# Optimization experiments

Measured on AMD Instinct MI355X. Metric: run time of the kernel, lower is better.

The kernel has to match this reference:

```python
import jax, jax.numpy as jnp
import numpy as np
import math

EPS = 1e-5

def _ln(x, g, b):
    m = jnp.mean(x, axis=-1, keepdims=True)
    v = jnp.mean((x - m) ** 2, axis=-1, keepdims=True)
    return (x - m) * jax.lax.rsqrt(v + EPS) * g + b

def _heads(t, H):
    B, T, C = t.shape
    return t.reshape(B, T, H, C // H).transpose(0, 2, 1, 3)  # [B,H,T,D]

def _merge(t):
    B, H, T, D = t.shape
    return t.transpose(0, 2, 1, 3).reshape(B, T, H * D)

def _self_attn(x, w, b, pw, pb, H):
    B, T, C = x.shape
    q, k, v = jnp.split(x @ w + b, 3, axis=-1)
    q, k, v = _heads(q, H), _heads(k, H), _heads(v, H)
    D = C // H
    att = jnp.einsum('bhqd,bhkd->bhqk', q, k) * (1.0 / math.sqrt(D))
    causal = jnp.tril(jnp.ones((T, T), bool))
    att = jnp.where(causal[None, None], att, jnp.float32(-jnp.inf))
    att = jax.nn.softmax(att, axis=-1)
    out = _merge(jnp.einsum('bhqk,bhkd->bhqd', att, v))
    return out @ pw + pb

def _cross_attn(enc, dec, w, b, pw, pb, H):
    B, Td, C = dec.shape
    q_dec = jnp.split(dec @ w + b, 3, axis=-1)[0]
    _, k_enc, v_enc = jnp.split(enc @ w + b, 3, axis=-1)
    q = _heads(q_dec, H); k = _heads(k_enc, H); v = _heads(v_enc, H)
    D = C // H
    att = jnp.einsum('bhqd,bhkd->bhqk', q, k) * (1.0 / math.sqrt(D))
    att = jax.nn.softmax(att, axis=-1)
    out = _merge(jnp.einsum('bhqk,bhkd->bhqd', att, v))
    return out @ pw + pb

def _block(x, encoder_embd,
           ln1_g, ln1_b, ln2_g, ln2_b, ln3_g, ln3_b,
           attn_w, attn_b, aproj_w, aproj_b,
           ca_w, ca_b, caproj_w, caproj_b,
           fc_w, fc_b, mproj_w, mproj_b,
           down_w, down_b, up_w, up_b, H=16):
    x = x + _self_attn(_ln(x, ln1_g, ln1_b), attn_w, attn_b, aproj_w, aproj_b, H)
    x = x + _cross_attn(encoder_embd, _ln(x, ln2_g, ln2_b), ca_w, ca_b, caproj_w, caproj_b, H)
    h = jax.nn.gelu(_ln(x, ln3_g, ln3_b) @ fc_w + fc_b, approximate=True) @ mproj_w + mproj_b
    adapt = jax.nn.gelu(h @ down_w + down_b, approximate=True) @ up_w + up_b + h  # Adapter residual
    return x + adapt


def setup_inputs() -> dict:
    key = jax.random.key(0)
    ks = jax.random.split(key, 12)
    B, T, Te, C, H = 4, 1024, 257, 1024, 16
    s = 0.02
    f32 = jnp.float32
    return {
        'x': jax.random.normal(ks[0], (B, T, C), f32),
        'encoder_embd': jax.random.normal(ks[1], (B, Te, C), f32),
        'prefix_embd': jnp.zeros((B, 1, C), f32),
        'ln1_g': jnp.ones((C,), f32), 'ln1_b': jnp.zeros((C,), f32),
        'ln2_g': jnp.ones((C,), f32), 'ln2_b': jnp.zeros((C,), f32),
        'ln3_g': jnp.ones((C,), f32), 'ln3_b': jnp.zeros((C,), f32),
        'attn_w': jax.random.normal(ks[2], (C, 3 * C), f32) * s,
        'attn_b': jnp.zeros((3 * C,), f32),
        'aproj_w': jax.random.normal(ks[3], (C, C), f32) * s,
        'aproj_b': jnp.zeros((C,), f32),
        'ca_w': jax.random.normal(ks[4], (C, 3 * C), f32) * s,
        'ca_b': jnp.zeros((3 * C,), f32),
        'caproj_w': jax.random.normal(ks[5], (C, C), f32) * s,
        'caproj_b': jnp.zeros((C,), f32),
        'fc_w': jax.random.normal(ks[6], (C, 4 * C), f32) * s,
        'fc_b': jnp.zeros((4 * C,), f32),
        'mproj_w': jax.random.normal(ks[7], (4 * C, C), f32) * s,
        'mproj_b': jnp.zeros((C,), f32),
        'down_w': jax.random.normal(ks[8], (C, C // 4), f32) * s,
        'down_b': jnp.zeros((C // 4,), f32),
        'up_w': jax.random.normal(ks[9], (C // 4, C), f32) * s,
        'up_b': jnp.zeros((C,), f32),
    }


def reference(x, encoder_embd, prefix_embd,
              ln1_g, ln1_b, ln2_g, ln2_b, ln3_g, ln3_b,
              attn_w, attn_b, aproj_w, aproj_b,
              ca_w, ca_b, caproj_w, caproj_b,
              fc_w, fc_b, mproj_w, mproj_b,
              down_w, down_b, up_w, up_b):
    # prefix_embd unused (peft='adapter')
    return _block(x, encoder_embd,
                  ln1_g, ln1_b, ln2_g, ln2_b, ln3_g, ln3_b,
                  attn_w, attn_b, aproj_w, aproj_b,
                  ca_w, ca_b, caproj_w, caproj_b,
                  fc_w, fc_b, mproj_w, mproj_b,
                  down_w, down_b, up_w, up_b)
```

## Files before the change

kernel.cpp:

```cpp
#include <hip/hip_runtime.h>

typedef __attribute__((ext_vector_type(8))) short short8v;
typedef __attribute__((ext_vector_type(8))) unsigned short ushort8v;
typedef __attribute__((ext_vector_type(4))) float f32x4;

__device__ __forceinline__ unsigned short f2b(float f) {
  unsigned int u = __float_as_uint(f);
  unsigned int r = (u + 0x7FFFu + ((u >> 16) & 1u)) >> 16;
  return (unsigned short)r;
}
__device__ __forceinline__ float b2f(unsigned short h) {
  return __uint_as_float(((unsigned int)h) << 16);
}
__device__ __forceinline__ float gelu_f(float x) {
  float z = 0.7978845608028654f * (x + 0.044715f * x * x * x);
  float e = __expf(2.0f * z);
  float t = 1.0f - 2.0f / (e + 1.0f);
  return 0.5f * x * (1.0f + t);
}
__device__ __forceinline__ void gload16(const void* g, void* l) {
  __builtin_amdgcn_global_load_lds((const __attribute__((address_space(1))) unsigned int*)g,
                                   (__attribute__((address_space(3))) unsigned int*)l,
                                   16, 0, 0);
}

__global__ __launch_bounds__(256) void k_transpose_cvt(const float* __restrict__ w,
                                                       unsigned short* __restrict__ wt,
                                                       int K, int N) {
  __shared__ float tile[64][65];
  int tn = blockIdx.x * 64, tk = blockIdx.y * 64;
  int c = threadIdx.x & 63, r0 = threadIdx.x >> 6;
#pragma unroll
  for (int p = 0; p < 16; ++p) {
    int r = r0 + p * 4;
    tile[r][c] = w[(size_t)(tk + r) * N + tn + c];
  }
  __syncthreads();
#pragma unroll
  for (int p = 0; p < 16; ++p) {
    int r = r0 + p * 4;
    wt[(size_t)(tn + r) * K + tk + c] = f2b(tile[c][r]);
  }
}

__global__ void k_cvt_bf16(const float* __restrict__ in, unsigned short* __restrict__ out, int n) {
  int i = blockIdx.x * 256 + threadIdx.x;
  if (i < n) out[i] = f2b(in[i]);
}

__global__ __launch_bounds__(256) void k_ln(const float* __restrict__ in,
                                            const float* __restrict__ g,
                                            const float* __restrict__ b,
                                            unsigned short* __restrict__ out) {
  int row = blockIdx.x;
  const float* x = in + (size_t)row * 1024;
  int t = threadIdx.x;
  float v0 = x[t], v1 = x[t + 256], v2 = x[t + 512], v3 = x[t + 768];
  float s = v0 + v1 + v2 + v3;
  float s2 = v0 * v0 + v1 * v1 + v2 * v2 + v3 * v3;
#pragma unroll
  for (int m = 1; m < 64; m <<= 1) { s += __shfl_xor(s, m); s2 += __shfl_xor(s2, m); }
  __shared__ float rs[4], rs2[4];
  int w = t >> 6;
  if ((t & 63) == 0) { rs[w] = s; rs2[w] = s2; }
  __syncthreads();
  s = rs[0] + rs[1] + rs[2] + rs[3];
  s2 = rs2[0] + rs2[1] + rs2[2] + rs2[3];
  float mean = s * (1.0f / 1024.0f);
  float var = s2 * (1.0f / 1024.0f) - mean * mean;
  float rinv = rsqrtf(var + 1e-5f);
  unsigned short* o = out + (size_t)row * 1024;
  o[t]       = f2b((v0 - mean) * rinv * g[t]       + b[t]);
  o[t + 256] = f2b((v1 - mean) * rinv * g[t + 256] + b[t + 256]);
  o[t + 512] = f2b((v2 - mean) * rinv * g[t + 512] + b[t + 512]);
  o[t + 768] = f2b((v3 - mean) * rinv * g[t + 768] + b[t + 768]);
}

template <bool GELU>
__global__ __launch_bounds__(512, 2) void k_g256(
    const unsigned short* __restrict__ A, int lda,
    const unsigned short* __restrict__ W, int ldw,
    const float* __restrict__ bias,
    unsigned short* __restrict__ outB, int ldo, int K) {
  __shared__ unsigned short lds[65536];
  const int t = threadIdx.x;
  const int tileM = blockIdx.y * 256, tileN = blockIdx.x * 256;
  const int lane = t & 63, w = t >> 6;
  const int wm = w >> 2, wn = w & 3;
  const int lr16 = lane & 15, kc4 = lane >> 4;

  const int row1 = t >> 2, row2 = row1 + 128, cs = t & 3;
  const int c1 = (cs ^ ((row1 >> 1) & 3)) * 8;
  const int c2 = (cs ^ ((row2 >> 1) & 3)) * 8;
  const unsigned short* a1 = A + (size_t)(tileM + row1) * lda + c1;
  const unsigned short* a2 = A + (size_t)(tileM + row2) * lda + c2;
  const unsigned short* w1 = W + (size_t)(tileN + row1) * ldw + c1;
  const unsigned short* w2 = W + (size_t)(tileN + row2) * ldw + c2;

  f32x4 acc[8][4];
#pragma unroll
  for (int i = 0; i < 8; ++i)
#pragma unroll
    for (int j = 0; j < 4; ++j) acc[i][j] = f32x4{0.f, 0.f, 0.f, 0.f};

  const int nt = K >> 6;

#define STAGE256(b, koff)                                  \
  do {                                                     \
    unsigned short* dst = &lds[(b) * 32768 + t * 8];       \
    gload16(a1 + (koff), dst);                             \
    gload16(a2 + (koff), dst + 4096);                      \
    gload16(a1 + (koff) + 32, dst + 8192);                 \
    gload16(a2 + (koff) + 32, dst + 12288);                \
    gload16(w1 + (koff), dst + 16384);                     \
    gload16(w2 + (koff), dst + 20480);                     \
    gload16(w1 + (koff) + 32, dst + 24576);                \
    gload16(w2 + (koff) + 32, dst + 28672);                \
  } while (0)

  STAGE256(0, 0);
  asm volatile("s_waitcnt vmcnt(0)" ::: "memory");
  __builtin_amdgcn_s_barrier();

  for (int T = 0; T < nt; ++T) {
    if (T + 1 < nt) STAGE256((T + 1) & 1, (T + 1) * 64);
    const unsigned short* buf = &lds[(T & 1) * 32768];
#pragma unroll
    for (int s = 0; s < 2; ++s) {
      const unsigned short* ab = buf + s * 8192;
      const unsigned short* bb = buf + 16384 + s * 8192;
      short8v bfr[4];
#pragma unroll
      for (int n = 0; n < 4; ++n) {
        int r = wn * 64 + n * 16 + lr16;
        bfr[n] = *(const short8v*)&bb[r * 32 + (kc4 ^ ((r >> 1) & 3)) * 8];
      }
#pragma unroll
      for (int mi = 0; mi < 8; ++mi) {
        int r = wm * 128 + mi * 16 + lr16;
        short8v af = *(const short8v*)&ab[r * 32 + (kc4 ^ ((r >> 1) & 3)) * 8];
#pragma unroll
        for (int n = 0; n < 4; ++n)
          acc[mi][n] = __builtin_amdgcn_mfma_f32_16x16x32_bf16(af, bfr[n], acc[mi][n], 0, 0, 0);
      }
    }
    if (T + 1 < nt) {
      asm volatile("s_waitcnt vmcnt(0)" ::: "memory");
      __builtin_amdgcn_s_barrier();
    }
  }
#undef STAGE256

#pragma unroll
  for (int mi = 0; mi < 8; ++mi) {
#pragma unroll
    for (int n = 0; n < 4; ++n) {
      int col = tileN + wn * 64 + n * 16 + lr16;
      float bv = bias[col];
#pragma unroll
      for (int qi = 0; qi < 4; ++qi) {
        int row = tileM + wm * 128 + mi * 16 + kc4 * 4 + qi;
        float v = acc[mi][n][qi] + bv;
        if (GELU) v = gelu_f(v);
        outB[(size_t)row * ldo + col] = f2b(v);
      }
    }
  }
}

template <bool GELU, bool WF32, bool WBF16, int NRES>
__global__ __launch_bounds__(256) void k_g128(
    const unsigned short* __restrict__ A, int lda,
    const unsigned short* __restrict__ W, int ldw,
    const float* __restrict__ bias,
    const float* __restrict__ res1, const float* __restrict__ res2,
    float* __restrict__ outF, unsigned short* __restrict__ outB,
    int M, int N, int K) {
  __shared__ unsigned short lds[32768];
  const int t = threadIdx.x;
  const int tileM = blockIdx.y * 128, tileN = blockIdx.x * 128;
  const int lane = t & 63, w = t >> 6;
  const int wm = (w >> 1) * 64, wn = (w & 1) * 64;
  const int lr16 = lane & 15, kc4 = lane >> 4;

  const int row1 = t >> 2, row2 = row1 + 64, cs = t & 3;
  const int c1 = (cs ^ ((row1 >> 1) & 3)) * 8;
  const int c2 = (cs ^ ((row2 >> 1) & 3)) * 8;
  int gr1 = tileM + row1; if (gr1 >= M) gr1 = M - 1;
  int gr2 = tileM + row2; if (gr2 >= M) gr2 = M - 1;
  const unsigned short* a1 = A + (size_t)gr1 * lda + c1;
  const unsigned short* a2 = A + (size_t)gr2 * lda + c2;
  const unsigned short* w1 = W + (size_t)(tileN + row1) * ldw + c1;
  const unsigned short* w2 = W + (size_t)(tileN + row2) * ldw + c2;

  f32x4 acc[4][4];
#pragma unroll
  for (int i = 0; i < 4; ++i)
#pragma unroll
    for (int j = 0; j < 4; ++j) acc[i][j] = f32x4{0.f, 0.f, 0.f, 0.f};

  const int nt = K >> 6;

#define STAGE128(b, koff)                                  \
  do {                                                     \
    unsigned short* dst = &lds[(b) * 16384 + t * 8];       \
    gload16(a1 + (koff), dst);                             \
    gload16(a2 + (koff), dst + 2048);                      \
    gload16(a1 + (koff) + 32, dst + 4096);                 \
    gload16(a2 + (koff) + 32, dst + 6144);                 \
    gload16(w1 + (koff), dst + 8192);                      \
    gload16(w2 + (koff), dst + 10240);                     \
    gload16(w1 + (koff) + 32, dst + 12288);                \
    gload16(w2 + (koff) + 32, dst + 14336);                \
  } while (0)

  STAGE128(0, 0);
  asm volatile("s_waitcnt vmcnt(0)" ::: "memory");
  __builtin_amdgcn_s_barrier();

  for (int T = 0; T < nt; ++T) {
    if (T + 1 < nt) STAGE128((T + 1) & 1, (T + 1) * 64);
    const unsigned short* buf = &lds[(T & 1) * 16384];
#pragma unroll
    for (int s = 0; s < 2; ++s) {
      const unsigned short* ab = buf + s * 4096;
      const unsigned short* bb = buf + 8192 + s * 4096;
      short8v bfr[4];
#pragma unroll
      for (int n = 0; n < 4; ++n) {
        int r = wn + n * 16 + lr16;
        bfr[n] = *(const short8v*)&bb[r * 32 + (kc4 ^ ((r >> 1) & 3)) * 8];
      }
#pragma unroll
      for (int mi = 0; mi < 4; ++mi) {
        int r = wm + mi * 16 + lr16;
        short8v af = *(const short8v*)&ab[r * 32 + (kc4 ^ ((r >> 1) & 3)) * 8];
#pragma unroll
        for (int n = 0; n < 4; ++n)
          acc[mi][n] = __builtin_amdgcn_mfma_f32_16x16x32_bf16(af, bfr[n], acc[mi][n], 0, 0, 0);
      }
    }
    if (T + 1 < nt) {
      asm volatile("s_waitcnt vmcnt(0)" ::: "memory");
      __builtin_amdgcn_s_barrier();
    }
  }
#undef STAGE128

#pragma unroll
  for (int mi = 0; mi < 4; ++mi) {
#pragma unroll
    for (int n = 0; n < 4; ++n) {
      int col = tileN + wn + n * 16 + lr16;
      float bv = bias[col];
#pragma unroll
      for (int qi = 0; qi < 4; ++qi) {
        int row = tileM + wm + mi * 16 + kc4 * 4 + qi;
        if (row < M) {
          float v = acc[mi][n][qi] + bv;
          if (GELU) v = gelu_f(v);
          size_t o = (size_t)row * N + col;
          if (NRES >= 1) v += res1[o];
          if (NRES >= 2) v += res2[o];
          if (WF32) outF[o] = v;
          if (WBF16) outB[o] = f2b(v);
        }
      }
    }
  }
}

__global__ __launch_bounds__(256) void k_vtrans(const unsigned short* __restrict__ src,
                                                int src_stride, int src_off, int TB,
                                                unsigned short* __restrict__ dst, int dst_tstride) {
  __shared__ unsigned short tile[64][72];
  int tb = blockIdx.x, bh = blockIdx.y;
  int b = bh >> 4, h = bh & 15;
  int t = threadIdx.x;
  int r = t >> 2, c0 = (t & 3) * 16;
  int tok = tb * 64 + r; if (tok >= TB) tok = TB - 1;
  const unsigned short* s = src + (size_t)(b * TB + tok) * src_stride + src_off + h * 64 + c0;
  *(ushort8v*)&tile[r][c0] = *(const ushort8v*)s;
  *(ushort8v*)&tile[r][c0 + 8] = *(const ushort8v*)(s + 8);
  __syncthreads();
  unsigned short tmp[16];
#pragma unroll
  for (int j = 0; j < 16; ++j) tmp[j] = tile[c0 + j][r];
  unsigned short* dp = dst + ((size_t)bh * 64 + r) * dst_tstride + tb * 64 + c0;
  *(ushort8v*)dp = *(const ushort8v*)&tmp[0];
  *(ushort8v*)(dp + 8) = *(const ushort8v*)&tmp[8];
}

template <bool CAUSAL>
__global__ __launch_bounds__(256) void k_attn(
    const unsigned short* __restrict__ Qb, int q_stride,
    const unsigned short* __restrict__ Kb, int k_stride, int k_off, int TKR,
    const unsigned short* __restrict__ Vt, int vt_tstride,
    unsigned short* __restrict__ out, int Tk) {
  __shared__ unsigned short Kl[64 * 72];
  __shared__ unsigned short Vl[64 * 72];
  __shared__ unsigned short Pl[4][16 * 72];
  int qb = blockIdx.x, bh = blockIdx.y;
  int b = bh >> 4, h = bh & 15;
  int t = threadIdx.x, lane = t & 63, w = t >> 6;
  int g = lane >> 4, lc = lane & 15;

  int qrow_g = qb * 64 + w * 16 + lc;
  const unsigned short* qp = Qb + (size_t)(b * 1024 + qrow_g) * q_stride + h * 64 + g * 8;
  short8v aq0 = *(const short8v*)qp;
  short8v aq1 = *(const short8v*)(qp + 32);

  f32x4 o[4];
  float m_[4], l_[4];
#pragma unroll
  for (int dt = 0; dt < 4; ++dt) o[dt] = f32x4{0.f, 0.f, 0.f, 0.f};
#pragma unroll
  for (int r = 0; r < 4; ++r) { m_[r] = -3.0e38f; l_[r] = 0.0f; }

  int srow = t >> 2;
  int sc = (t & 3) * 16;
  int ntiles = CAUSAL ? (qb + 1) : ((Tk + 63) >> 6);

  for (int kt = 0; kt < ntiles; ++kt) {
    __syncthreads();
    {
      int kg = kt * 64 + srow;
      if (!CAUSAL && kg >= Tk) kg = Tk - 1;
      const unsigned short* ks = Kb + (size_t)(b * TKR + kg) * k_stride + k_off + h * 64 + sc;
      *(ushort8v*)&Kl[srow * 72 + sc]     = *(const ushort8v*)ks;
      *(ushort8v*)&Kl[srow * 72 + sc + 8] = *(const ushort8v*)(ks + 8);
      const unsigned short* vs = Vt + ((size_t)bh * 64 + srow) * vt_tstride + kt * 64 + sc;
      *(ushort8v*)&Vl[srow * 72 + sc]     = *(const ushort8v*)vs;
      *(ushort8v*)&Vl[srow * 72 + sc + 8] = *(const ushort8v*)(vs + 8);
    }
    __syncthreads();

    f32x4 s[4];
#pragma unroll
    for (int jt = 0; jt < 4; ++jt) {
      short8v bk0 = *(const short8v*)&Kl[(jt * 16 + lc) * 72 + g * 8];
      short8v bk1 = *(const short8v*)&Kl[(jt * 16 + lc) * 72 + g * 8 + 32];
      f32x4 acc = f32x4{0.f, 0.f, 0.f, 0.f};
      acc = __builtin_amdgcn_mfma_f32_16x16x32_bf16(aq0, bk0, acc, 0, 0, 0);
      acc = __builtin_amdgcn_mfma_f32_16x16x32_bf16(aq1, bk1, acc, 0, 0, 0);
      s[jt] = acc;
    }
#pragma unroll
    for (int jt = 0; jt < 4; ++jt)
#pragma unroll
      for (int r = 0; r < 4; ++r) {
        float sv = s[jt][r] * 0.125f;
        bool masked = CAUSAL ? (kt == qb && (jt * 16 + lc) > (w * 16 + g * 4 + r))
                             : (kt * 64 + jt * 16 + lc >= Tk);
        s[jt][r] = masked ? -3.0e38f : sv;
      }
    float f[4];
#pragma unroll
    for (int r = 0; r < 4; ++r) {
      float mx = fmaxf(fmaxf(s[0][r], s[1][r]), fmaxf(s[2][r], s[3][r]));
      mx = fmaxf(mx, __shfl_xor(mx, 1));
      mx = fmaxf(mx, __shfl_xor(mx, 2));
      mx = fmaxf(mx, __shfl_xor(mx, 4));
      mx = fmaxf(mx, __shfl_xor(mx, 8));
      float mnew = fmaxf(m_[r], mx);
      f[r] = __expf(m_[r] - mnew);
      m_[r] = mnew;
      float rsum = 0.0f;
#pragma unroll
      for (int jt = 0; jt < 4; ++jt) {
        float p = __expf(s[jt][r] - mnew);
        s[jt][r] = p;
        rsum += p;
      }
      rsum += __shfl_xor(rsum, 1);
      rsum += __shfl_xor(rsum, 2);
      rsum += __shfl_xor(rsum, 4);
      rsum += __shfl_xor(rsum, 8);
      l_[r] = l_[r] * f[r] + rsum;
    }
#pragma unroll
    for (int dt = 0; dt < 4; ++dt)
#pragma unroll
      for (int r = 0; r < 4; ++r) o[dt][r] *= f[r];
#pragma unroll
    for (int jt = 0; jt < 4; ++jt)
#pragma unroll
      for (int r = 0; r < 4; ++r)
        Pl[w][(g * 4 + r) * 72 + jt * 16 + lc] = f2b(s[jt][r]);
    short8v ap0 = *(const short8v*)&Pl[w][lc * 72 + g * 8];
    short8v ap1 = *(const short8v*)&Pl[w][lc * 72 + g * 8 + 32];
#pragma unroll
    for (int dt = 0; dt < 4; ++dt) {
      short8v bv0 = *(const short8v*)&Vl[(dt * 16 + lc) * 72 + g * 8];
      short8v bv1 = *(const short8v*)&Vl[(dt * 16 + lc) * 72 + g * 8 + 32];
      o[dt] = __builtin_amdgcn_mfma_f32_16x16x32_bf16(ap0, bv0, o[dt], 0, 0, 0);
      o[dt] = __builtin_amdgcn_mfma_f32_16x16x32_bf16(ap1, bv1, o[dt], 0, 0, 0);
    }
  }
  size_t orow = (size_t)(b * 1024 + qb * 64 + w * 16) * 1024 + h * 64;
#pragma unroll
  for (int r = 0; r < 4; ++r) {
    float inv = 1.0f / l_[r];
#pragma unroll
    for (int dt = 0; dt < 4; ++dt)
      out[orow + (size_t)(g * 4 + r) * 1024 + dt * 16 + lc] = f2b(o[dt][r] * inv);
  }
}

extern "C" void kernel_launch(void* const* d_in, const int* in_sizes, int n_in,
                              void* d_out, int out_size, void* d_ws, size_t ws_size,
                              hipStream_t stream) {
  (void)in_sizes; (void)n_in; (void)out_size; (void)ws_size;
  const float* x       = (const float*)d_in[0];
  const float* enc     = (const float*)d_in[1];
  const float* ln1_g   = (const float*)d_in[3];
  const float* ln1_b   = (const float*)d_in[4];
  const float* ln2_g   = (const float*)d_in[5];
  const float* ln2_b   = (const float*)d_in[6];
  const float* ln3_g   = (const float*)d_in[7];
  const float* ln3_b   = (const float*)d_in[8];
  const float* attn_w  = (const float*)d_in[9];
  const float* attn_b  = (const float*)d_in[10];
  const float* aproj_w = (const float*)d_in[11];
  const float* aproj_b = (const float*)d_in[12];
  const float* ca_w    = (const float*)d_in[13];
  const float* ca_b    = (const float*)d_in[14];
  const float* caproj_w= (const float*)d_in[15];
  const float* caproj_b= (const float*)d_in[16];
  const float* fc_w    = (const float*)d_in[17];
  const float* fc_b    = (const float*)d_in[18];
  const float* mproj_w = (const float*)d_in[19];
  const float* mproj_b = (const float*)d_in[20];
  const float* down_w  = (const float*)d_in[21];
  const float* down_b  = (const float*)d_in[22];
  const float* up_w    = (const float*)d_in[23];
  const float* up_b    = (const float*)d_in[24];
  float* out = (float*)d_out;
  char* ws = (char*)d_ws;

  const size_t O_WATTN = 0, O_WAPROJ = 6291456, O_WCA = 8388608, O_WCAPROJ = 14680064,
               O_WFC = 16777216, O_WMPROJ = 25165824, O_WDOWN = 33554432, O_WUP = 34078720,
               O_ENC = 34603008, O_LN = 36708352, O_BIG = 45096960,
               O_XRES = 78651392, O_HF = 95428608, O_ATTN = 112205824;

  unsigned short* wt_attn   = (unsigned short*)(ws + O_WATTN);
  unsigned short* wt_aproj  = (unsigned short*)(ws + O_WAPROJ);
  unsigned short* wt_ca     = (unsigned short*)(ws + O_WCA);
  unsigned short* wt_caproj = (unsigned short*)(ws + O_WCAPROJ);
  unsigned short* wt_fc     = (unsigned short*)(ws + O_WFC);
  unsigned short* wt_mproj  = (unsigned short*)(ws + O_WMPROJ);
  unsigned short* wt_down   = (unsigned short*)(ws + O_WDOWN);
  unsigned short* wt_up     = (unsigned short*)(ws + O_WUP);
  unsigned short* encbf     = (unsigned short*)(ws + O_ENC);
  unsigned short* lnout     = (unsigned short*)(ws + O_LN);
  unsigned short* hbf       = (unsigned short*)(ws + O_LN);
  unsigned short* qkvb      = (unsigned short*)(ws + O_BIG);
  unsigned short* vt_self   = (unsigned short*)(ws + O_BIG + 25165824);
  unsigned short* q2b       = (unsigned short*)(ws + O_BIG);
  unsigned short* kvb       = (unsigned short*)(ws + O_BIG + 8388608);
  unsigned short* vt_cross  = (unsigned short*)(ws + O_BIG + 12599296);
  unsigned short* caout     = (unsigned short*)(ws + O_BIG + 15220736);
  unsigned short* fcout     = (unsigned short*)(ws + O_BIG);
  float*          xres      = (float*)(ws + O_XRES);
  float*          hf        = (float*)(ws + O_HF);
  unsigned short* attnout   = (unsigned short*)(ws + O_ATTN);
  unsigned short* dmid      = (unsigned short*)(ws + O_ATTN);

  dim3 blk(256);
  dim3 blk5(512);

  k_transpose_cvt<<<dim3(48, 16), blk, 0, stream>>>(attn_w,  wt_attn,   1024, 3072);
  k_transpose_cvt<<<dim3(16, 16), blk, 0, stream>>>(aproj_w, wt_aproj,  1024, 1024);
  k_transpose_cvt<<<dim3(48, 16), blk, 0, stream>>>(ca_w,    wt_ca,     1024, 3072);
  k_transpose_cvt<<<dim3(16, 16), blk, 0, stream>>>(caproj_w,wt_caproj, 1024, 1024);
  k_transpose_cvt<<<dim3(64, 16), blk, 0, stream>>>(fc_w,    wt_fc,     1024, 4096);
  k_transpose_cvt<<<dim3(16, 64), blk, 0, stream>>>(mproj_w, wt_mproj,  4096, 1024);
  k_transpose_cvt<<<dim3(4, 16),  blk, 0, stream>>>(down_w,  wt_down,   1024, 256);
  k_transpose_cvt<<<dim3(16, 4),  blk, 0, stream>>>(up_w,    wt_up,     256,  1024);
  k_cvt_bf16<<<dim3(4112), blk, 0, stream>>>(enc, encbf, 1028 * 1024);

  k_ln<<<dim3(4096), blk, 0, stream>>>(x, ln1_g, ln1_b, lnout);
  k_g256<false><<<dim3(12, 16), blk5, 0, stream>>>(
      lnout, 1024, wt_attn, 1024, attn_b, qkvb, 3072, 1024);
  k_vtrans<<<dim3(16, 64), blk, 0, stream>>>(qkvb, 3072, 2048, 1024, vt_self, 1024);
  k_attn<true><<<dim3(16, 64), blk, 0, stream>>>(
      qkvb, 3072, qkvb, 3072, 1024, 1024, vt_self, 1024, attnout, 1024);
  k_g128<false, true, false, 1><<<dim3(8, 32), blk, 0, stream>>>(
      attnout, 1024, wt_aproj, 1024, aproj_b, x, nullptr, xres, nullptr, 4096, 1024, 1024);

  k_ln<<<dim3(4096), blk, 0, stream>>>(xres, ln2_g, ln2_b, lnout);
  k_g128<false, false, true, 0><<<dim3(8, 32), blk, 0, stream>>>(
      lnout, 1024, wt_ca, 1024, ca_b, nullptr, nullptr, nullptr, q2b, 4096, 1024, 1024);
  k_g128<false, false, true, 0><<<dim3(16, 9), blk, 0, stream>>>(
      encbf, 1024, wt_ca + (size_t)1024 * 1024, 1024, ca_b + 1024, nullptr, nullptr,
      nullptr, kvb, 1028, 2048, 1024);
  k_vtrans<<<dim3(5, 64), blk, 0, stream>>>(kvb, 2048, 1024, 257, vt_cross, 320);
  k_attn<false><<<dim3(16, 64), blk, 0, stream>>>(
      q2b, 1024, kvb, 2048, 0, 257, vt_cross, 320, caout, 257);
  k_g128<false, true, false, 1><<<dim3(8, 32), blk, 0, stream>>>(
      caout, 1024, wt_caproj, 1024, caproj_b, xres, nullptr, xres, nullptr, 4096, 1024, 1024);

  k_ln<<<dim3(4096), blk, 0, stream>>>(xres, ln3_g, ln3_b, lnout);
  k_g256<true><<<dim3(16, 16), blk5, 0, stream>>>(
      lnout, 1024, wt_fc, 1024, fc_b, fcout, 4096, 1024);
  k_g128<false, true, true, 0><<<dim3(8, 32), blk, 0, stream>>>(
      fcout, 4096, wt_mproj, 4096, mproj_b, nullptr, nullptr, hf, hbf, 4096, 1024, 4096);

  k_g128<true, false, true, 0><<<dim3(2, 32), blk, 0, stream>>>(
      hbf, 1024, wt_down, 1024, down_b, nullptr, nullptr, nullptr, dmid, 4096, 256, 1024);
  k_g128<false, true, false, 2><<<dim3(8, 32), blk, 0, stream>>>(
      dmid, 256, wt_up, 256, up_b, hf, xres, out, nullptr, 4096, 1024, 256);
}
```

Measured before the change: 504.9 us.

## Deepen k_g256 pipeline to half-tile stages and drop fp32 h buffer

```diff
diff --git a/kernel.cpp b/kernel.cpp
--- a/kernel.cpp
+++ b/kernel.cpp
@@ -77,7 +77,7 @@
 }
 
 template <bool GELU>
-__global__ __launch_bounds__(512, 2) void k_g256(
+__global__ __launch_bounds__(512, 2) void k_g256p(
     const unsigned short* __restrict__ A, int lda,
     const unsigned short* __restrict__ W, int ldw,
     const float* __restrict__ bias,
@@ -104,52 +104,67 @@
     for (int j = 0; j < 4; ++j) acc[i][j] = f32x4{0.f, 0.f, 0.f, 0.f};
 
   const int nt = K >> 6;
-
-#define STAGE256(b, koff)                                  \
-  do {                                                     \
-    unsigned short* dst = &lds[(b) * 32768 + t * 8];       \
-    gload16(a1 + (koff), dst);                             \
-    gload16(a2 + (koff), dst + 4096);                      \
-    gload16(a1 + (koff) + 32, dst + 8192);                 \
-    gload16(a2 + (koff) + 32, dst + 12288);                \
-    gload16(w1 + (koff), dst + 16384);                     \
-    gload16(w2 + (koff), dst + 20480);                     \
-    gload16(w1 + (koff) + 32, dst + 24576);                \
-    gload16(w2 + (koff) + 32, dst + 28672);                \
+  const int H = nt * 4;
+
+#define STAGE_HALF(h)                                                        \
+  do {                                                                       \
+    int tile_s = (h) >> 2, id = (h) & 3, slot = (h) & 7;                     \
+    int koff = tile_s * 64 + (id >> 1) * 32;                                 \
+    unsigned short* dst = &lds[slot * 8192 + t * 8];                         \
+    if (id & 1) { gload16(w1 + koff, dst); gload16(w2 + koff, dst + 4096); } \
+    else        { gload16(a1 + koff, dst); gload16(a2 + koff, dst + 4096); } \
   } while (0)
 
-  STAGE256(0, 0);
-  asm volatile("s_waitcnt vmcnt(0)" ::: "memory");
+#pragma unroll
+  for (int h = 0; h < 6; ++h) { if (h < H) STAGE_HALF(h); }
+  asm volatile("s_waitcnt vmcnt(8)" ::: "memory");
   __builtin_amdgcn_s_barrier();
 
   for (int T = 0; T < nt; ++T) {
-    if (T + 1 < nt) STAGE256((T + 1) & 1, (T + 1) * 64);
-    const unsigned short* buf = &lds[(T & 1) * 32768];
-#pragma unroll
-    for (int s = 0; s < 2; ++s) {
-      const unsigned short* ab = buf + s * 8192;
-      const unsigned short* bb = buf + 16384 + s * 8192;
-      short8v bfr[4];
-#pragma unroll
-      for (int n = 0; n < 4; ++n) {
-        int r = wn * 64 + n * 16 + lr16;
-        bfr[n] = *(const short8v*)&bb[r * 32 + (kc4 ^ ((r >> 1) & 3)) * 8];
-      }
-#pragma unroll
-      for (int mi = 0; mi < 8; ++mi) {
-        int r = wm * 128 + mi * 16 + lr16;
-        short8v af = *(const short8v*)&ab[r * 32 + (kc4 ^ ((r >> 1) & 3)) * 8];
+    short8v bfr[4];
+#pragma unroll
+    for (int q = 0; q < 4; ++q) {
+      const int ks = q >> 1, mh = q & 1;
+      const int aslot = (((T & 1) * 4 + 2 * ks)) * 8192;
+      const int bslot = (((T & 1) * 4 + 2 * ks + 1)) * 8192;
+      if (mh == 0) {
+#pragma unroll
+        for (int n = 0; n < 4; ++n) {
+          int r = wn * 64 + n * 16 + lr16;
+          bfr[n] = *(const short8v*)&lds[bslot + r * 32 + (kc4 ^ ((r >> 1) & 3)) * 8];
+        }
+      }
+      short8v aF[4];
+#pragma unroll
+      for (int m4 = 0; m4 < 4; ++m4) {
+        int r = wm * 128 + mh * 64 + m4 * 16 + lr16;
+        aF[m4] = *(const short8v*)&lds[aslot + r * 32 + (kc4 ^ ((r >> 1) & 3)) * 8];
+      }
+      int h = 4 * T + q + 6;
+      if (h < H) STAGE_HALF(h);
+      if (q & 1) {
+        if (T < nt - 2)       asm volatile("s_waitcnt vmcnt(8)" ::: "memory");
+        else if (T == nt - 2) {
+          if (q == 1)         asm volatile("s_waitcnt vmcnt(4)" ::: "memory");
+          else                asm volatile("s_waitcnt vmcnt(0)" ::: "memory");
+        }
+      }
+      __builtin_amdgcn_s_barrier();
+      asm volatile("s_waitcnt lgkmcnt(0)" ::: "memory");
+      __builtin_amdgcn_sched_barrier(0);
+      __builtin_amdgcn_s_setprio(1);
+#pragma unroll
+      for (int m4 = 0; m4 < 4; ++m4)
 #pragma unroll
         for (int n = 0; n < 4; ++n)
-          acc[mi][n] = __builtin_amdgcn_mfma_f32_16x16x32_bf16(af, bfr[n], acc[mi][n], 0, 0, 0);
-      }
-    }
-    if (T + 1 < nt) {
-      asm volatile("s_waitcnt vmcnt(0)" ::: "memory");
+          acc[mh * 4 + m4][n] =
+              __builtin_amdgcn_mfma_f32_16x16x32_bf16(aF[m4], bfr[n], acc[mh * 4 + m4][n], 0, 0, 0);
+      __builtin_amdgcn_s_setprio(0);
+      __builtin_amdgcn_sched_barrier(0);
       __builtin_amdgcn_s_barrier();
     }
   }
-#undef STAGE256
+#undef STAGE_HALF
 
 #pragma unroll
   for (int mi = 0; mi < 8; ++mi) {
@@ -168,12 +183,13 @@
   }
 }
 
-template <bool GELU, bool WF32, bool WBF16, int NRES>
+template <bool GELU, bool WF32, bool WBF16, int NRES, bool RES1B>
 __global__ __launch_bounds__(256) void k_g128(
     const unsigned short* __restrict__ A, int lda,
     const unsigned short* __restrict__ W, int ldw,
     const float* __restrict__ bias,
-    const float* __restrict__ res1, const float* __restrict__ res2,
+    const float* __restrict__ res1, const unsigned short* __restrict__ res1b,
+    const float* __restrict__ res2,
     float* __restrict__ outF, unsigned short* __restrict__ outB,
     int M, int N, int K) {
   __shared__ unsigned short lds[32768];
@@ -260,7 +276,7 @@
           float v = acc[mi][n][qi] + bv;
           if (GELU) v = gelu_f(v);
           size_t o = (size_t)row * N + col;
-          if (NRES >= 1) v += res1[o];
+          if (NRES >= 1) v += RES1B ? b2f(res1b[o]) : res1[o];
           if (NRES >= 2) v += res2[o];
           if (WF32) outF[o] = v;
           if (WBF16) outB[o] = f2b(v);
@@ -441,7 +457,7 @@
   const size_t O_WATTN = 0, O_WAPROJ = 6291456, O_WCA = 8388608, O_WCAPROJ = 14680064,
                O_WFC = 16777216, O_WMPROJ = 25165824, O_WDOWN = 33554432, O_WUP = 34078720,
                O_ENC = 34603008, O_LN = 36708352, O_BIG = 45096960,
-               O_XRES = 78651392, O_HF = 95428608, O_ATTN = 112205824;
+               O_XRES = 78651392, O_ATTN = 112205824;
 
   unsigned short* wt_attn   = (unsigned short*)(ws + O_WATTN);
   unsigned short* wt_aproj  = (unsigned short*)(ws + O_WAPROJ);
@@ -462,7 +478,6 @@
   unsigned short* caout     = (unsigned short*)(ws + O_BIG + 15220736);
   unsigned short* fcout     = (unsigned short*)(ws + O_BIG);
   float*          xres      = (float*)(ws + O_XRES);
-  float*          hf        = (float*)(ws + O_HF);
   unsigned short* attnout   = (unsigned short*)(ws + O_ATTN);
   unsigned short* dmid      = (unsigned short*)(ws + O_ATTN);
 
@@ -480,34 +495,40 @@
   k_cvt_bf16<<<dim3(4112), blk, 0, stream>>>(enc, encbf, 1028 * 1024);
 
   k_ln<<<dim3(4096), blk, 0, stream>>>(x, ln1_g, ln1_b, lnout);
-  k_g256<false><<<dim3(12, 16), blk5, 0, stream>>>(
+  k_g256p<false><<<dim3(12, 16), blk5, 0, stream>>>(
       lnout, 1024, wt_attn, 1024, attn_b, qkvb, 3072, 1024);
   k_vtrans<<<dim3(16, 64), blk, 0, stream>>>(qkvb, 3072, 2048, 1024, vt_self, 1024);
   k_attn<true><<<dim3(16, 64), blk, 0, stream>>>(
       qkvb, 3072, qkvb, 3072, 1024, 1024, vt_self, 1024, attnout, 1024);
-  k_g128<false, true, false, 1><<<dim3(8, 32), blk, 0, stream>>>(
-      attnout, 1024, wt_aproj, 1024, aproj_b, x, nullptr, xres, nullptr, 4096, 1024, 1024);
+  k_g128<false, true, false, 1, false><<<dim3(8, 32), blk, 0, stream>>>(
+      attnout, 1024, wt_aproj, 1024, aproj_b, x, nullptr, nullptr, xres, nullptr,
+      4096, 1024, 1024);
 
   k_ln<<<dim3(4096), blk, 0, stream>>>(xres, ln2_g, ln2_b, lnout);
-  k_g128<false, false, true, 0><<<dim3(8, 32), blk, 0, stream>>>(
-      lnout, 1024, wt_ca, 1024, ca_b, nullptr, nullptr, nullptr, q2b, 4096, 1024, 1024);
-  k_g128<false, false, true, 0><<<dim3(16, 9), blk, 0, stream>>>(
+  k_g128<false, false, true, 0, false><<<dim3(8, 32), blk, 0, stream>>>(
+      lnout, 1024, wt_ca, 1024, ca_b, nullptr, nullptr, nullptr, nullptr, q2b,
+      4096, 1024, 1024);
+  k_g128<false, false, true, 0, false><<<dim3(16, 9), blk, 0, stream>>>(
       encbf, 1024, wt_ca + (size_t)1024 * 1024, 1024, ca_b + 1024, nullptr, nullptr,
-      nullptr, kvb, 1028, 2048, 1024);
+      nullptr, nullptr, kvb, 1028, 2048, 1024);
   k_vtrans<<<dim3(5, 64), blk, 0, stream>>>(kvb, 2048, 1024, 257, vt_cross, 320);
   k_attn<false><<<dim3(16, 64), blk, 0, stream>>>(
       q2b, 1024, kvb, 2048, 0, 257, vt_cross, 320, caout, 257);
-  k_g128<false, true, false, 1><<<dim3(8, 32), blk, 0, stream>>>(
-      caout, 1024, wt_caproj, 1024, caproj_b, xres, nullptr, xres, nullptr, 4096, 1024, 1024);
+  k_g128<false, true, false, 1, false><<<dim3(8, 32), blk, 0, stream>>>(
+      caout, 1024, wt_caproj, 1024, caproj_b, xres, nullptr, nullptr, xres, nullptr,
+      4096, 1024, 1024);
 
   k_ln<<<dim3(4096), blk, 0, stream>>>(xres, ln3_g, ln3_b, lnout);
-  k_g256<true><<<dim3(16, 16), blk5, 0, stream>>>(
+  k_g256p<true><<<dim3(16, 16), blk5, 0, stream>>>(
       lnout, 1024, wt_fc, 1024, fc_b, fcout, 4096, 1024);
-  k_g128<false, true, true, 0><<<dim3(8, 32), blk, 0, stream>>>(
-      fcout, 4096, wt_mproj, 4096, mproj_b, nullptr, nullptr, hf, hbf, 4096, 1024, 4096);
-
-  k_g128<true, false, true, 0><<<dim3(2, 32), blk, 0, stream>>>(
-      hbf, 1024, wt_down, 1024, down_b, nullptr, nullptr, nullptr, dmid, 4096, 256, 1024);
-  k_g128<false, true, false, 2><<<dim3(8, 32), blk, 0, stream>>>(
-      dmid, 256, wt_up, 256, up_b, hf, xres, out, nullptr, 4096, 1024, 256);
-}
+  k_g128<false, false, true, 0, false><<<dim3(8, 32), blk, 0, stream>>>(
+      fcout, 4096, wt_mproj, 4096, mproj_b, nullptr, nullptr, nullptr, nullptr, hbf,
+      4096, 1024, 4096);
+
+  k_g128<true, false, true, 0, false><<<dim3(2, 32), blk, 0, stream>>>(
+      hbf, 1024, wt_down, 1024, down_b, nullptr, nullptr, nullptr, nullptr, dmid,
+      4096, 256, 1024);
+  k_g128<false, true, false, 2, true><<<dim3(8, 32), blk, 0, stream>>>(
+      dmid, 256, wt_up, 256, up_b, nullptr, hbf, xres, out, nullptr,
+      4096, 1024, 256);
+}
```

Measured after the change: 498.9 us. No clear change (-1.2%).
